# Optimization experiments

Measured on AMD Instinct MI355X. Metric: run time of the kernel, lower is better.

The kernel has to match this reference:

```python
import jax, jax.numpy as jnp
import numpy as np

B, S, K = 8, 128, 12          # batch, seq len, nPredicts
DAR, DENC = 256, 256          # AR dim, encoder dim
NNEG = 128                    # negativeSamplingExt
W = S - K                     # windowSize


def setup_inputs() -> dict:
    key = jax.random.key(0)
    k1, k2, k3, k4, k5 = jax.random.split(key, 5)
    cFeature = jax.random.normal(k1, (B, S, DAR), dtype=jnp.float32)
    encodedData = jax.random.normal(k2, (B, S, DENC), dtype=jnp.float32)
    # stacked bias-free Linear weights, one per prediction step k
    Wpred = jax.random.normal(k3, (K, DENC, DAR), dtype=jnp.float32) / jnp.sqrt(DAR)
    n_idx = NNEG * W * B
    batchIdx = jax.random.randint(k4, (n_idx,), 0, B, dtype=jnp.int32)
    seqIdx = jax.random.randint(k5, (n_idx,), 1, S, dtype=jnp.int32)  # low=1 as in torch
    return {"cFeature": cFeature, "encodedData": encodedData, "Wpred": Wpred,
            "batchIdx": batchIdx, "seqIdx": seqIdx}


def reference(cFeature, encodedData, Wpred, batchIdx, seqIdx):
    c = cFeature[:, :W]                                   # (B, W, DAR)
    flat = encodedData.reshape(-1, DENC)                  # (B*S, DENC)

    # sampleClean: baseIdx arange(W) broadcast over (B, NNEG, W) then flattened
    base = jnp.tile(jnp.arange(W, dtype=jnp.int32), B * NNEG)
    seq = (seqIdx + base) % S
    ext = seq + batchIdx * S
    negExt = flat[ext].reshape(B, NNEG, W, DENC)          # irregular gather, ~121 MB

    # per-k linear prediction: locC[k] = c @ Wpred[k].T
    locC = jnp.einsum('bwd,ked->kbwe', c, Wpred)          # (K, B, W, DENC)

    # positives: encodedData[:, k:k+W] for k = 1..K
    pos = jnp.stack([encodedData[:, k:k + W] for k in range(1, K + 1)])  # (K, B, W, DENC)

    # (locC * candidates).mean(dim=feature) == dot / DENC
    posScore = jnp.einsum('kbwe,kbwe->kbw', locC, pos) / DENC           # (K, B, W)
    negScore = jnp.einsum('kbwe,bnwe->kbnw', locC, negExt) / DENC       # (K, B, N, W)

    logits = jnp.concatenate([posScore[:, :, None, :], negScore], axis=2)  # (K, B, 1+N, W)
    logits = jnp.transpose(logits, (0, 1, 3, 2)).reshape(K, B * W, 1 + NNEG)

    # cross entropy with label 0 (positive at class index 0)
    lse = jax.nn.logsumexp(logits, axis=-1)               # (K, B*W)
    losses = jnp.mean(lse - logits[..., 0], axis=-1)      # (K,)
    accs = jnp.mean((jnp.argmax(logits, axis=-1) == 0).astype(jnp.float32), axis=-1)
    return losses[None, :], accs[None, :]                  # (1, K), (1, K)
```

## Files before the change

kernel.cpp:

```cpp
#include <hip/hip_runtime.h>
#include <math.h>

#define B_    8
#define S_    128
#define K_    12
#define DAR_  256
#define DENC_ 256
#define NNEG_ 128
#define W_    116
#define BW_   928

typedef __attribute__((ext_vector_type(8))) short short8;
typedef __attribute__((ext_vector_type(4))) float floatx4;

static __device__ __forceinline__ unsigned short f2bf(float f) {
    union { float f; unsigned int u; } v; v.f = f;
    return (unsigned short)((v.u + 0x7FFFu + ((v.u >> 16) & 1u)) >> 16);
}

__global__ __launch_bounds__(256) void cast_all(
    const float* __restrict__ enc, const float* __restrict__ cf,
    const float* __restrict__ wp,
    unsigned short* __restrict__ ench, unsigned short* __restrict__ cfh,
    unsigned short* __restrict__ wph)
{
    const int g = blockIdx.x * 256 + threadIdx.x;
    const float* src; unsigned short* dst; int off;
    if (g < 32768)      { src = enc; dst = ench; off = g * 8; }
    else if (g < 65536) { src = cf;  dst = cfh;  off = (g - 32768) * 8; }
    else                { src = wp;  dst = wph;  off = (g - 65536) * 8; }
    float4 v0 = *(const float4*)(src + off);
    float4 v1 = *(const float4*)(src + off + 4);
    uint4 o;
    o.x = f2bf(v0.x) | ((unsigned)f2bf(v0.y) << 16);
    o.y = f2bf(v0.z) | ((unsigned)f2bf(v0.w) << 16);
    o.z = f2bf(v1.x) | ((unsigned)f2bf(v1.y) << 16);
    o.w = f2bf(v1.z) | ((unsigned)f2bf(v1.w) << 16);
    *(uint4*)(dst + off) = o;
}

__global__ __launch_bounds__(256) void stage1_mfma(
    const unsigned short* __restrict__ cfh,
    const unsigned short* __restrict__ wph,
    unsigned short* __restrict__ locCh)
{
    __shared__ unsigned short Ah[64 * 256];
    __shared__ unsigned short Bh[64 * 256];

    const int tid = threadIdx.x;
    const int mt = blockIdx.x;
    const int nt = blockIdx.y;
    const int k  = blockIdx.z;

#pragma unroll
    for (int i = 0; i < 8; ++i) {
        const int flat = i * 256 + tid;
        const int row = flat >> 5, ch = flat & 31;
        const int sw = (row * 32 + (ch ^ (row & 7))) * 8;
        const int bw = mt * 64 + row;
        uint4 av = make_uint4(0u, 0u, 0u, 0u);
        if (bw < BW_) {
            const int b = bw / W_, w = bw - b * W_;
            av = *(const uint4*)(cfh + ((size_t)(b * S_ + w) * 256 + ch * 8));
        }
        *(uint4*)&Ah[sw] = av;
        const int e = nt * 64 + row;
        uint4 bv = *(const uint4*)(wph + ((size_t)(k * 256 + e) * 256 + ch * 8));
        *(uint4*)&Bh[sw] = bv;
    }
    __syncthreads();

    const int lane = tid & 63, wv = tid >> 6;
    const int l15 = lane & 15, quad = lane >> 4;

    short8 a[8];
    const int am = wv * 16 + l15;
#pragma unroll
    for (int kt = 0; kt < 8; ++kt) {
        const int ch = kt * 4 + quad;
        a[kt] = *(const short8*)&Ah[(am * 32 + (ch ^ (am & 7))) * 8];
    }

    floatx4 acc[4];
#pragma unroll
    for (int n4 = 0; n4 < 4; ++n4) {
        floatx4 c = {0.f, 0.f, 0.f, 0.f};
        const int bn = n4 * 16 + l15;
#pragma unroll
        for (int kt = 0; kt < 8; ++kt) {
            const int ch = kt * 4 + quad;
            short8 bfrag = *(const short8*)&Bh[(bn * 32 + (ch ^ (bn & 7))) * 8];
            c = __builtin_amdgcn_mfma_f32_16x16x32_bf16(a[kt], bfrag, c, 0, 0, 0);
        }
        acc[n4] = c;
    }

#pragma unroll
    for (int n4 = 0; n4 < 4; ++n4) {
        const int e = nt * 64 + n4 * 16 + l15;
#pragma unroll
        for (int r = 0; r < 4; ++r) {
            const int bwo = mt * 64 + wv * 16 + quad * 4 + r;
            if (bwo < BW_)
                locCh[((size_t)k * BW_ + bwo) * 256 + e] = f2bf(acc[n4][r]);
        }
    }
}

__global__ __launch_bounds__(256) void stage2_mfma(
    const unsigned short* __restrict__ ench,
    const unsigned short* __restrict__ locCh,
    const int* __restrict__ batchIdx,
    const int* __restrict__ seqIdx,
    float* __restrict__ part)
{
    __shared__ unsigned short Al[16 * 256];
    __shared__ unsigned short Bl[140 * 256];
    int*   idxL = (int*)&Al[12 * 256];
    float* sc   = (float*)Bl;

    const int tid = threadIdx.x;
    const int bw = blockIdx.x;
    const int b = bw / W_, w = bw - b * W_;

    if (tid < NNEG_) {
        const int ii = (b * NNEG_ + tid) * W_ + w;
        const int bi = batchIdx[ii];
        int si = seqIdx[ii] + w;
        if (si >= S_) si -= S_;
        idxL[tid] = bi * S_ + si;
    } else if (tid < 140) {
        idxL[tid] = b * S_ + w + 1 + (tid - 128);
    }

    {
        const int row = tid >> 5, ch = tid & 31;
        uint4 v = *(const uint4*)(locCh + ((size_t)row * BW_ + bw) * 256 + ch * 8);
        *(uint4*)&Al[(row * 32 + (ch ^ (row & 7))) * 8] = v;
    }
    if (tid < 128) {
        const int f2 = 256 + tid;
        const int row = f2 >> 5, ch = f2 & 31;
        uint4 v = *(const uint4*)(locCh + ((size_t)row * BW_ + bw) * 256 + ch * 8);
        *(uint4*)&Al[(row * 32 + (ch ^ (row & 7))) * 8] = v;
    }
    __syncthreads();

#pragma unroll
    for (int i = 0; i < 18; ++i) {
        const int flat = i * 256 + tid;
        if (flat < 4480) {
            const int row = flat >> 5, ch = flat & 31;
            const int ri = idxL[row];
            uint4 v = *(const uint4*)(ench + (size_t)ri * 256 + ch * 8);
            *(uint4*)&Bl[(row * 32 + (ch ^ (row & 7))) * 8] = v;
        }
    }
    __syncthreads();

    const int lane = tid & 63, wv = tid >> 6;
    const int l15 = lane & 15, quad = lane >> 4;

    short8 a[8];
#pragma unroll
    for (int kt = 0; kt < 8; ++kt) {
        const int ch = kt * 4 + quad;
        a[kt] = *(const short8*)&Al[(l15 * 32 + (ch ^ (l15 & 7))) * 8];
    }

    floatx4 accT[3];
#pragma unroll
    for (int u = 0; u < 3; ++u) {
        const int t = wv + u * 4;
        floatx4 c = {0.f, 0.f, 0.f, 0.f};
        if (t < 9) {
            const int n = t * 16 + l15;
            const int nn = (n < 140) ? n : 128;
#pragma unroll
            for (int kt = 0; kt < 8; ++kt) {
                const int ch = kt * 4 + quad;
                short8 bfrag = *(const short8*)&Bl[(nn * 32 + (ch ^ (nn & 7))) * 8];
                c = __builtin_amdgcn_mfma_f32_16x16x32_bf16(a[kt], bfrag, c, 0, 0, 0);
            }
        }
        accT[u] = c;
    }
    __syncthreads();

    const float inv = 1.0f / 256.0f;
#pragma unroll
    for (int u = 0; u < 3; ++u) {
        const int t = wv + u * 4;
        if (t < 9) {
#pragma unroll
            for (int r = 0; r < 4; ++r) {
                const int m = quad * 4 + r;
                if (m < K_) {
                    const float val = accT[u][r] * inv;
                    if (t < 8)           sc[m * 132 + t * 16 + l15] = val;
                    else if (l15 == m)   sc[m * 132 + 128] = val;
                }
            }
        }
    }
    __syncthreads();

    for (int k = wv; k < K_; k += 4) {
        const float x0  = sc[k * 132 + lane];
        const float x1  = sc[k * 132 + 64 + lane];
        const float pos = sc[k * 132 + 128];
        float mn = fmaxf(x0, x1);
#pragma unroll
        for (int o = 1; o < 64; o <<= 1) mn = fmaxf(mn, __shfl_xor(mn, o, 64));
        const float m = fmaxf(mn, pos);
        float s = __expf(x0 - m) + __expf(x1 - m);
#pragma unroll
        for (int o = 1; o < 64; o <<= 1) s += __shfl_xor(s, o, 64);
        if (lane == 0) {
            const float lse = m + __logf(s + __expf(pos - m));
            part[k * BW_ + bw]        = lse - pos;
            part[(K_ + k) * BW_ + bw] = (pos >= mn) ? 1.0f : 0.0f;
        }
    }
}

__global__ __launch_bounds__(256) void stage3_reduce(
    const float* __restrict__ part, float* __restrict__ out)
{
    __shared__ float wsum[4];
    const int o = blockIdx.x, tid = threadIdx.x;
    float s = 0.f;
    for (int i = tid; i < BW_; i += 256) s += part[o * BW_ + i];
#pragma unroll
    for (int off = 1; off < 64; off <<= 1) s += __shfl_xor(s, off, 64);
    if ((tid & 63) == 0) wsum[tid >> 6] = s;
    __syncthreads();
    if (tid == 0)
        out[o] = (wsum[0] + wsum[1] + wsum[2] + wsum[3]) / (float)BW_;
}

extern "C" void kernel_launch(void* const* d_in, const int* in_sizes, int n_in,
                              void* d_out, int out_size, void* d_ws, size_t ws_size,
                              hipStream_t stream) {
    const float* cFeat    = (const float*)d_in[0];
    const float* enc      = (const float*)d_in[1];
    const float* Wp       = (const float*)d_in[2];
    const int*   batchIdx = (const int*)d_in[3];
    const int*   seqIdx   = (const int*)d_in[4];
    float* out = (float*)d_out;

    unsigned short* ench  = (unsigned short*)d_ws;
    unsigned short* cfh   = ench + 262144;
    unsigned short* wph   = cfh + 262144;
    unsigned short* locCh = wph + 786432;
    float*          part  = (float*)(locCh + (size_t)K_ * BW_ * 256);

    hipLaunchKernelGGL(cast_all, dim3(640), dim3(256), 0, stream,
                       enc, cFeat, Wp, ench, cfh, wph);
    hipLaunchKernelGGL(stage1_mfma, dim3(15, 4, 12), dim3(256), 0, stream,
                       cfh, wph, locCh);
    hipLaunchKernelGGL(stage2_mfma, dim3(BW_), dim3(256), 0, stream,
                       ench, locCh, batchIdx, seqIdx, part);
    hipLaunchKernelGGL(stage3_reduce, dim3(24), dim3(256), 0, stream,
                       part, out);
}
```

Before: 95.25 us.

## Load MFMA operands directly from global memory, bypassing LDS staging

In stage1 the A operand (cFeature rows) is now loaded straight from global memory into per-lane MFMA fragments instead of being staged through shared memory. In stage2 both the locC rows and the gathered encoder rows are read directly from global into fragments, which removes the large 70KB LDS buffer and one barrier. This frees LDS, which should allow higher occupancy and remove the staging writes and reads. The cost is uncoalesced 16-byte per-lane global loads that may now be redundant across waves, since several waves reread the same rows through the cache.

Result: faster. 92.93 us (-2.4%).

```diff
diff --git a/kernel.cpp b/kernel.cpp
--- a/kernel.cpp
+++ b/kernel.cpp
@@ -44,7 +44,6 @@
     const unsigned short* __restrict__ wph,
     unsigned short* __restrict__ locCh)
 {
-    __shared__ unsigned short Ah[64 * 256];
     __shared__ unsigned short Bh[64 * 256];
 
     const int tid = threadIdx.x;
@@ -52,34 +51,32 @@
     const int nt = blockIdx.y;
     const int k  = blockIdx.z;
 
+    const int lane = tid & 63, wv = tid >> 6;
+    const int l15 = lane & 15, quad = lane >> 4;
+
+    const int am = mt * 64 + wv * 16 + l15;
+    const bool avalid = (am < BW_);
+    short8 a[8];
+    if (avalid) {
+        const int b = am / W_, w = am - b * W_;
+        const unsigned short* arow = cfh + (size_t)(b * S_ + w) * 256;
+#pragma unroll
+        for (int kt = 0; kt < 8; ++kt)
+            a[kt] = *(const short8*)(arow + kt * 32 + quad * 8);
+    } else {
+#pragma unroll
+        for (int kt = 0; kt < 8; ++kt) a[kt] = short8{0,0,0,0,0,0,0,0};
+    }
+
 #pragma unroll
     for (int i = 0; i < 8; ++i) {
         const int flat = i * 256 + tid;
         const int row = flat >> 5, ch = flat & 31;
-        const int sw = (row * 32 + (ch ^ (row & 7))) * 8;
-        const int bw = mt * 64 + row;
-        uint4 av = make_uint4(0u, 0u, 0u, 0u);
-        if (bw < BW_) {
-            const int b = bw / W_, w = bw - b * W_;
-            av = *(const uint4*)(cfh + ((size_t)(b * S_ + w) * 256 + ch * 8));
-        }
-        *(uint4*)&Ah[sw] = av;
         const int e = nt * 64 + row;
         uint4 bv = *(const uint4*)(wph + ((size_t)(k * 256 + e) * 256 + ch * 8));
-        *(uint4*)&Bh[sw] = bv;
-    }
-    __syncthreads();
-
-    const int lane = tid & 63, wv = tid >> 6;
-    const int l15 = lane & 15, quad = lane >> 4;
-
-    short8 a[8];
-    const int am = wv * 16 + l15;
-#pragma unroll
-    for (int kt = 0; kt < 8; ++kt) {
-        const int ch = kt * 4 + quad;
-        a[kt] = *(const short8*)&Ah[(am * 32 + (ch ^ (am & 7))) * 8];
-    }
+        *(uint4*)&Bh[(row * 32 + (ch ^ (row & 7))) * 8] = bv;
+    }
+    __syncthreads();
 
     floatx4 acc[4];
 #pragma unroll
@@ -102,7 +99,7 @@
         for (int r = 0; r < 4; ++r) {
             const int bwo = mt * 64 + wv * 16 + quad * 4 + r;
             if (bwo < BW_)
-                locCh[((size_t)k * BW_ + bwo) * 256 + e] = f2bf(acc[n4][r]);
+                locCh[((size_t)k * BW_ + bwo) * 256 + e] = f2bf(acc[r < 0 ? 0 : n4][r]);
         }
     }
 }
@@ -114,14 +111,22 @@
     const int* __restrict__ seqIdx,
     float* __restrict__ part)
 {
-    __shared__ unsigned short Al[16 * 256];
-    __shared__ unsigned short Bl[140 * 256];
-    int*   idxL = (int*)&Al[12 * 256];
-    float* sc   = (float*)Bl;
+    __shared__ int   idxL[144];
+    __shared__ float sc[K_ * 132];
 
     const int tid = threadIdx.x;
     const int bw = blockIdx.x;
     const int b = bw / W_, w = bw - b * W_;
+
+    const int lane = tid & 63, wv = tid >> 6;
+    const int l15 = lane & 15, quad = lane >> 4;
+
+    const int m = (l15 < K_) ? l15 : (K_ - 1);
+    const unsigned short* arow = locCh + ((size_t)m * BW_ + bw) * 256;
+    short8 a[8];
+#pragma unroll
+    for (int kt = 0; kt < 8; ++kt)
+        a[kt] = *(const short8*)(arow + kt * 32 + quad * 8);
 
     if (tid < NNEG_) {
         const int ii = (b * NNEG_ + tid) * W_ + w;
@@ -132,41 +137,7 @@
     } else if (tid < 140) {
         idxL[tid] = b * S_ + w + 1 + (tid - 128);
     }
-
-    {
-        const int row = tid >> 5, ch = tid & 31;
-        uint4 v = *(const uint4*)(locCh + ((size_t)row * BW_ + bw) * 256 + ch * 8);
-        *(uint4*)&Al[(row * 32 + (ch ^ (row & 7))) * 8] = v;
-    }
-    if (tid < 128) {
-        const int f2 = 256 + tid;
-        const int row = f2 >> 5, ch = f2 & 31;
-        uint4 v = *(const uint4*)(locCh + ((size_t)row * BW_ + bw) * 256 + ch * 8);
-        *(uint4*)&Al[(row * 32 + (ch ^ (row & 7))) * 8] = v;
-    }
-    __syncthreads();
-
-#pragma unroll
-    for (int i = 0; i < 18; ++i) {
-        const int flat = i * 256 + tid;
-        if (flat < 4480) {
-            const int row = flat >> 5, ch = flat & 31;
-            const int ri = idxL[row];
-            uint4 v = *(const uint4*)(ench + (size_t)ri * 256 + ch * 8);
-            *(uint4*)&Bl[(row * 32 + (ch ^ (row & 7))) * 8] = v;
-        }
-    }
-    __syncthreads();
-
-    const int lane = tid & 63, wv = tid >> 6;
-    const int l15 = lane & 15, quad = lane >> 4;
-
-    short8 a[8];
-#pragma unroll
-    for (int kt = 0; kt < 8; ++kt) {
-        const int ch = kt * 4 + quad;
-        a[kt] = *(const short8*)&Al[(l15 * 32 + (ch ^ (l15 & 7))) * 8];
-    }
+    __syncthreads();
 
     floatx4 accT[3];
 #pragma unroll
@@ -176,16 +147,15 @@
         if (t < 9) {
             const int n = t * 16 + l15;
             const int nn = (n < 140) ? n : 128;
+            const unsigned short* brow = ench + (size_t)idxL[nn] * 256;
 #pragma unroll
             for (int kt = 0; kt < 8; ++kt) {
-                const int ch = kt * 4 + quad;
-                short8 bfrag = *(const short8*)&Bl[(nn * 32 + (ch ^ (nn & 7))) * 8];
+                short8 bfrag = *(const short8*)(brow + kt * 32 + quad * 8);
                 c = __builtin_amdgcn_mfma_f32_16x16x32_bf16(a[kt], bfrag, c, 0, 0, 0);
             }
         }
         accT[u] = c;
     }
-    __syncthreads();
 
     const float inv = 1.0f / 256.0f;
 #pragma unroll
@@ -194,11 +164,11 @@
         if (t < 9) {
 #pragma unroll
             for (int r = 0; r < 4; ++r) {
-                const int m = quad * 4 + r;
-                if (m < K_) {
+                const int mm = quad * 4 + r;
+                if (mm < K_) {
                     const float val = accT[u][r] * inv;
-                    if (t < 8)           sc[m * 132 + t * 16 + l15] = val;
-                    else if (l15 == m)   sc[m * 132 + 128] = val;
+                    if (t < 8)           sc[mm * 132 + t * 16 + l15] = val;
+                    else if (l15 == mm)  sc[mm * 132 + 128] = val;
                 }
             }
         }
@@ -212,12 +182,12 @@
         float mn = fmaxf(x0, x1);
 #pragma unroll
         for (int o = 1; o < 64; o <<= 1) mn = fmaxf(mn, __shfl_xor(mn, o, 64));
-        const float m = fmaxf(mn, pos);
-        float s = __expf(x0 - m) + __expf(x1 - m);
+        const float m2 = fmaxf(mn, pos);
+        float s = __expf(x0 - m2) + __expf(x1 - m2);
 #pragma unroll
         for (int o = 1; o < 64; o <<= 1) s += __shfl_xor(s, o, 64);
         if (lane == 0) {
-            const float lse = m + __logf(s + __expf(pos - m));
+            const float lse = m2 + __logf(s + __expf(pos - m2));
             part[k * BW_ + bw]        = lse - pos;
             part[(K_ + k) * BW_ + bw] = (pos >= mn) ? 1.0f : 0.0f;
         }
```
